# Kernel tuning notes

Hardware: AMD Instinct MI355X
Metric: run time of the kernel (lower is better)

The kernel has to match this reference:

```python
import jax, jax.numpy as jnp
import numpy as np

D_MODEL = 1024
N_HEADS = 16
D_HEAD = D_MODEL // N_HEADS
RANK = 256
N_COMPRESS = 64
N_EXPAND = 64
N_KNOWLEDGE = 4096
K_COMPRESS = 16
K_EXPAND = 8
K_KNOW = 8


def setup_inputs() -> dict:
    key = jax.random.key(0)
    ks = jax.random.split(key, 13)
    B, S = 8, 1024
    x = jax.random.normal(ks[0], (B, S, D_MODEL), dtype=jnp.float32)
    u = jax.random.uniform(ks[1], (B, S), dtype=jnp.float32)
    importance = u / jnp.sum(u, axis=-1, keepdims=True)  # token importance weights
    s = 0.02
    compress_w = jax.random.normal(ks[2], (N_COMPRESS, D_MODEL)) * s
    expQ_w = jax.random.normal(ks[3], (N_EXPAND, D_MODEL)) * s
    expK_w = jax.random.normal(ks[4], (N_EXPAND, D_MODEL)) * s
    expV_w = jax.random.normal(ks[5], (N_EXPAND, D_MODEL)) * s
    memory_w = jax.random.normal(ks[6], (N_COMPRESS, D_MODEL)) * s
    compress_neurons = jax.random.normal(ks[7], (N_COMPRESS, D_MODEL, RANK)) / jnp.sqrt(D_MODEL)
    expand_pool = jax.random.normal(ks[8], (N_EXPAND, RANK, D_MODEL)) / jnp.sqrt(RANK)
    knowledge_K = jax.random.normal(ks[9], (N_KNOWLEDGE, RANK)) * s
    knowledge_V = jax.random.normal(ks[10], (N_KNOWLEDGE, D_MODEL)) * s
    Wo = jax.random.normal(ks[11], (D_MODEL, D_MODEL)) / jnp.sqrt(D_MODEL)
    return dict(x=x, importance=importance, compress_w=compress_w, expQ_w=expQ_w,
                expK_w=expK_w, expV_w=expV_w, memory_w=memory_w,
                compress_neurons=compress_neurons, expand_pool=expand_pool,
                knowledge_K=knowledge_K, knowledge_V=knowledge_V, Wo=Wo)


def _route(x, importance, w_lin, k):
    # softmax router pref [B,S,N], importance-weighted sum -> [B,N], renorm, top-k renorm
    pref = jax.nn.softmax(jnp.einsum('bsd,nd->bsn', x, w_lin), axis=-1)
    w = jnp.einsum('bs,bsn->bn', importance, pref)
    w = w / (jnp.sum(w, axis=-1, keepdims=True) + 1e-8)
    tw, ti = jax.lax.top_k(w, k)
    tw = tw / (jnp.sum(tw, axis=-1, keepdims=True) + 1e-8)
    return tw, ti


def _forward(x, importance, compress_w, expQ_w, expK_w, expV_w, memory_w,
             compress_neurons, expand_pool, knowledge_K, knowledge_V, Wo):
    B, S, D = x.shape
    # ---- attention routing ----
    cw, ci = _route(x, importance, compress_w, K_COMPRESS)
    shared_c = jnp.einsum('bk,bkdr->bdr', cw, compress_neurons[ci])  # [B,D,R]
    h = jnp.einsum('bsd,bdr->bsr', x, shared_c)                      # [B,S,R]

    def expand(w_lin):
        ew, ei = _route(x, importance, w_lin, K_EXPAND)
        shared = jnp.einsum('bk,bkrd->brd', ew, expand_pool[ei])     # [B,R,D]
        return jnp.einsum('bsr,brd->bsd', h, shared)                 # [B,S,D]

    Q, K, V = expand(expQ_w), expand(expK_w), expand(expV_w)
    Qh = Q.reshape(B, S, N_HEADS, D_HEAD).transpose(0, 2, 1, 3)
    Kh = K.reshape(B, S, N_HEADS, D_HEAD).transpose(0, 2, 1, 3)
    Vh = V.reshape(B, S, N_HEADS, D_HEAD).transpose(0, 2, 1, 3)
    scores = jnp.einsum('bhqd,bhkd->bhqk', Qh, Kh) / jnp.sqrt(jnp.float32(D_HEAD))
    causal = jnp.tril(jnp.ones((S, S), dtype=bool))
    scores = jnp.where(causal, scores, jnp.float32(-1e30))
    attn = jax.nn.softmax(scores, axis=-1)
    out = jnp.einsum('bhqk,bhkd->bhqd', attn, Vh)
    out = out.transpose(0, 2, 1, 3).reshape(B, S, D)
    attn_out = jnp.einsum('bsd,ed->bse', out, Wo)

    # ---- memory routing (knowledge lookup) ----
    mw, mi = _route(x, importance, memory_w, K_COMPRESS)
    shared_m = jnp.einsum('bk,bkdr->bdr', mw, compress_neurons[mi])
    hm = jnp.einsum('bsd,bdr->bsr', x, shared_m)                     # [B,S,R]
    kscores = jnp.einsum('bsr,nr->bsn', hm, knowledge_K) / jnp.sqrt(jnp.float32(RANK))
    top_s, top_i = jax.lax.top_k(kscores, K_KNOW)                    # [B,S,k]
    p = jax.nn.softmax(top_s, axis=-1)
    mem_out = jnp.einsum('bsk,bskd->bsd', p, knowledge_V[top_i])

    return attn_out + mem_out


def reference(x, importance, compress_w, expQ_w, expK_w, expV_w, memory_w,
              compress_neurons, expand_pool, knowledge_K, knowledge_V, Wo):
    return _forward(x, importance, compress_w, expQ_w, expK_w, expV_w, memory_w,
                    compress_neurons, expand_pool, knowledge_K, knowledge_V, Wo)
```

## Files before the change

### kernel.cpp

```cpp
#include <hip/hip_runtime.h>

#define Bn   8
#define Sn   1024
#define Dn   1024
#define Rn   256
#define NHn  16
#define DHn  64
#define NKn  4096
#define TOK  (Bn*Sn)
#define EPE  (Dn*Rn)
#define TDN  3072
#define BPAD 44

typedef __attribute__((ext_vector_type(8))) short short8;
typedef __attribute__((ext_vector_type(4))) short short4v;
typedef __attribute__((ext_vector_type(4))) float f32x4;
typedef __attribute__((ext_vector_type(4))) unsigned short ushort4v;
typedef unsigned short ush;

__device__ inline ush f2bf(float f) {
    union { float f; unsigned u; } v; v.f = f;
    unsigned r = v.u + 0x7fffu + ((v.u >> 16) & 1u);
    return (ush)(r >> 16);
}
__device__ inline float bf2f(ush h) {
    union { unsigned u; float f; } v; v.u = ((unsigned)h) << 16;
    return v.f;
}
__device__ inline void f2bf_split(float f, ush& hi, ush& lo) {
    hi = f2bf(f);
    lo = f2bf(f - bf2f(hi));
}
__device__ inline short8 cat8(short4v a, short4v b) {
    short8 r;
    r[0]=a[0]; r[1]=a[1]; r[2]=a[2]; r[3]=a[3];
    r[4]=b[0]; r[5]=b[1]; r[6]=b[2]; r[7]=b[3];
    return r;
}

__global__ __launch_bounds__(256) void convert3(
    const float* __restrict__ s0, ush* __restrict__ h0, ush* __restrict__ l0, long long n40,
    const float* __restrict__ s1, ush* __restrict__ h1, ush* __restrict__ l1, long long n41,
    const float* __restrict__ s2, ush* __restrict__ h2, ush* __restrict__ l2, long long n42)
{
    long long i = (long long)blockIdx.x*256 + threadIdx.x;
    const float* s; ush* h; ush* l;
    if (i < n40) { s = s0; h = h0; l = l0; }
    else if (i < n40 + n41) { i -= n40; s = s1; h = h1; l = l1; }
    else { i -= n40 + n41; if (i >= n42) return; s = s2; h = h2; l = l2; }
    float4 f = *(const float4*)&s[i*4];
    float vals[4] = {f.x, f.y, f.z, f.w};
    ushort4v hv, lv;
#pragma unroll
    for (int e = 0; e < 4; ++e) { ush a, b2; f2bf_split(vals[e], a, b2); hv[e] = a; lv[e] = b2; }
    *(ushort4v*)&h[i*4] = hv;
    *(ushort4v*)&l[i*4] = lv;
}

__global__ __launch_bounds__(256) void convert_w5(
    const float* __restrict__ w0, const float* __restrict__ w1,
    const float* __restrict__ w2, const float* __restrict__ w3,
    const float* __restrict__ w4, ush* __restrict__ hi, ush* __restrict__ lo)
{
    int y = blockIdx.y;
    const float* srcs[5] = {w0, w1, w2, w3, w4};
    const float* s = srcs[y];
    long long i = (long long)blockIdx.x*256 + threadIdx.x;
    float4 f = *(const float4*)&s[i*4];
    float vals[4] = {f.x, f.y, f.z, f.w};
    ushort4v hv, lv;
#pragma unroll
    for (int e = 0; e < 4; ++e) { ush a, b2; f2bf_split(vals[e], a, b2); hv[e] = a; lv[e] = b2; }
    size_t dst = (size_t)y*64*Dn + i*4;
    *(ushort4v*)&hi[dst] = hv;
    *(ushort4v*)&lo[dst] = lv;
}

__global__ __launch_bounds__(256) void gemm_pre(
    const ush* __restrict__ Ahi, const ush* __restrict__ Alo,
    const ush* __restrict__ Bhi, const ush* __restrict__ Blo,
    void* __restrict__ C0, void* __restrict__ C1,
    int M, int N, int K, long long sA, long long sB, long long sC,
    float alpha, int bTrans, int passes, int outMode, int gridSwap)
{
    Ahi += (size_t)blockIdx.z * sA;
    if (Alo) Alo += (size_t)blockIdx.z * sA;
    Bhi += (size_t)blockIdx.z * sB;
    if (Blo) Blo += (size_t)blockIdx.z * sB;
    __shared__ __align__(16) ush AsH[128][40];
    __shared__ __align__(16) ush AsL[128][40];
    __shared__ __align__(16) ush BsH[64][BPAD];
    __shared__ __align__(16) ush BsL[64][BPAD];
    int tid = threadIdx.x;
    int wave = tid >> 6, lane = tid & 63;
    int lr = lane & 15, lg = lane >> 4;
    int wm = (wave >> 1)*64, wn = (wave & 1)*32;
    int row0 = (gridSwap ? blockIdx.x : blockIdx.y)*128;
    int col0 = (gridSwap ? blockIdx.y : blockIdx.x)*64;

    f32x4 acc[4][2];
#pragma unroll
    for (int i = 0; i < 4; ++i)
#pragma unroll
        for (int j = 0; j < 2; ++j) acc[i][j] = (f32x4){0.f,0.f,0.f,0.f};

    for (int k0 = 0; k0 < K; k0 += 32) {
        __syncthreads();
#pragma unroll
        for (int g = 0; g < 2; ++g) {
            int idx = tid + g*256;
            int m2 = idx >> 2, kk = (idx & 3)*8;
            size_t so = (size_t)(row0 + m2)*K + k0 + kk;
            *(short8*)&AsH[m2][kk] = *(const short8*)&Ahi[so];
            if (passes >= 2) *(short8*)&AsL[m2][kk] = *(const short8*)&Alo[so];
        }
        if (!bTrans) {
            int n2 = tid >> 2, kk = (tid & 3)*8;
            size_t so = (size_t)(col0 + n2)*K + k0 + kk;
            *(short4v*)&BsH[n2][kk]     = *(const short4v*)&Bhi[so];
            *(short4v*)&BsH[n2][kk + 4] = *(const short4v*)&Bhi[so + 4];
            if (passes >= 3) {
                *(short4v*)&BsL[n2][kk]     = *(const short4v*)&Blo[so];
                *(short4v*)&BsL[n2][kk + 4] = *(const short4v*)&Blo[so + 4];
            }
        } else {
            int kk = tid >> 3, n0 = (tid & 7)*8;
            size_t so = (size_t)(k0 + kk)*N + col0 + n0;
            short8 wh = *(const short8*)&Bhi[so];
#pragma unroll
            for (int e = 0; e < 8; ++e) BsH[n0+e][kk] = (ush)wh[e];
            if (passes >= 3) {
                short8 wl = *(const short8*)&Blo[so];
#pragma unroll
                for (int e = 0; e < 8; ++e) BsL[n0+e][kk] = (ush)wl[e];
            }
        }
        __syncthreads();
        short8 afH[4], bfH[2];
#pragma unroll
        for (int i = 0; i < 4; ++i) afH[i] = *(const short8*)&AsH[wm + i*16 + lr][lg*8];
#pragma unroll
        for (int j = 0; j < 2; ++j)
            bfH[j] = cat8(*(const short4v*)&BsH[wn + j*16 + lr][lg*8],
                          *(const short4v*)&BsH[wn + j*16 + lr][lg*8 + 4]);
#pragma unroll
        for (int i = 0; i < 4; ++i)
#pragma unroll
            for (int j = 0; j < 2; ++j)
                acc[i][j] = __builtin_amdgcn_mfma_f32_16x16x32_bf16(afH[i], bfH[j], acc[i][j], 0, 0, 0);
        if (passes >= 2) {
            short8 afL[4];
#pragma unroll
            for (int i = 0; i < 4; ++i) afL[i] = *(const short8*)&AsL[wm + i*16 + lr][lg*8];
#pragma unroll
            for (int i = 0; i < 4; ++i)
#pragma unroll
                for (int j = 0; j < 2; ++j)
                    acc[i][j] = __builtin_amdgcn_mfma_f32_16x16x32_bf16(afL[i], bfH[j], acc[i][j], 0, 0, 0);
        }
        if (passes >= 3) {
            short8 bfL[2];
#pragma unroll
            for (int j = 0; j < 2; ++j)
                bfL[j] = cat8(*(const short4v*)&BsL[wn + j*16 + lr][lg*8],
                              *(const short4v*)&BsL[wn + j*16 + lr][lg*8 + 4]);
#pragma unroll
            for (int i = 0; i < 4; ++i)
#pragma unroll
                for (int j = 0; j < 2; ++j)
                    acc[i][j] = __builtin_amdgcn_mfma_f32_16x16x32_bf16(afH[i], bfL[j], acc[i][j], 0, 0, 0);
        }
    }
#pragma unroll
    for (int i = 0; i < 4; ++i)
#pragma unroll
        for (int j = 0; j < 2; ++j)
#pragma unroll
            for (int r = 0; r < 4; ++r) {
                size_t eo = (size_t)(row0 + wm + i*16 + lg*4 + r)*N + col0 + wn + j*16 + lr;
                float val = acc[i][j][r] * alpha;
                if (outMode == 0) {
                    ((float*)C0 + (size_t)blockIdx.z*sC)[eo] = val;
                } else if (outMode == 1) {
                    ((ush*)C0 + (size_t)blockIdx.z*sC)[eo] = f2bf(val);
                } else {
                    ush h, l; f2bf_split(val, h, l);
                    ((ush*)C0 + (size_t)blockIdx.z*sC)[eo] = h;
                    ((ush*)C1 + (size_t)blockIdx.z*sC)[eo] = l;
                }
            }
}

__global__ __launch_bounds__(256) void gemm64(
    const ush* __restrict__ Ahi, const ush* __restrict__ Alo,
    const ush* __restrict__ Bhi, const ush* __restrict__ Blo,
    void* __restrict__ C0, void* __restrict__ C1,
    void* __restrict__ C2, void* __restrict__ C3,
    int N, int K, long long sA, long long sB, long long sCL, long long sCR,
    float alpha, int bTrans, int passes, int mode)
{
    Ahi += (size_t)blockIdx.z * sA;
    if (Alo) Alo += (size_t)blockIdx.z * sA;
    Bhi += (size_t)blockIdx.z * sB;
    if (Blo) Blo += (size_t)blockIdx.z * sB;
    __shared__ __align__(16) ush AsH[64][40];
    __shared__ __align__(16) ush AsL[64][40];
    __shared__ __align__(16) ush BsH[64][BPAD];
    __shared__ __align__(16) ush BsL[64][BPAD];
    int tid = threadIdx.x;
    int wave = tid >> 6, lane = tid & 63;
    int lr = lane & 15, lg = lane >> 4;
    int wm = (wave >> 1)*32, wn = (wave & 1)*32;
    int row0 = blockIdx.y*64, col0 = blockIdx.x*64;

    f32x4 acc[2][2];
#pragma unroll
    for (int i = 0; i < 2; ++i)
#pragma unroll
        for (int j = 0; j < 2; ++j) acc[i][j] = (f32x4){0.f,0.f,0.f,0.f};

    for (int k0 = 0; k0 < K; k0 += 32) {
        __syncthreads();
        {
            int m2 = tid >> 2, kk = (tid & 3)*8;
            size_t so = (size_t)(row0 + m2)*K + k0 + kk;
            *(short8*)&AsH[m2][kk] = *(const short8*)&Ahi[so];
            if (passes >= 2) *(short8*)&AsL[m2][kk] = *(const short8*)&Alo[so];
        }
        if (!bTrans) {
            int n2 = tid >> 2, kk = (tid & 3)*8;
            size_t so = (size_t)(col0 + n2)*K + k0 + kk;
            *(short4v*)&BsH[n2][kk]     = *(const short4v*)&Bhi[so];
            *(short4v*)&BsH[n2][kk + 4] = *(const short4v*)&Bhi[so + 4];
            if (passes >= 3) {
                *(short4v*)&BsL[n2][kk]     = *(const short4v*)&Blo[so];
                *(short4v*)&BsL[n2][kk + 4] = *(const short4v*)&Blo[so + 4];
            }
        } else {
            int kk = tid >> 3, n0 = (tid & 7)*8;
            size_t so = (size_t)(k0 + kk)*N + col0 + n0;
            short8 wh = *(const short8*)&Bhi[so];
#pragma unroll
            for (int e = 0; e < 8; ++e) BsH[n0+e][kk] = (ush)wh[e];
            if (passes >= 3) {
                short8 wl = *(const short8*)&Blo[so];
#pragma unroll
                for (int e = 0; e < 8; ++e) BsL[n0+e][kk] = (ush)wl[e];
            }
        }
        __syncthreads();
        short8 afH[2], bfH[2];
#pragma unroll
        for (int i = 0; i < 2; ++i) afH[i] = *(const short8*)&AsH[wm + i*16 + lr][lg*8];
#pragma unroll
        for (int j = 0; j < 2; ++j)
            bfH[j] = cat8(*(const short4v*)&BsH[wn + j*16 + lr][lg*8],
                          *(const short4v*)&BsH[wn + j*16 + lr][lg*8 + 4]);
#pragma unroll
        for (int i = 0; i < 2; ++i)
#pragma unroll
            for (int j = 0; j < 2; ++j)
                acc[i][j] = __builtin_amdgcn_mfma_f32_16x16x32_bf16(afH[i], bfH[j], acc[i][j], 0, 0, 0);
        if (passes >= 2) {
            short8 afL[2];
#pragma unroll
            for (int i = 0; i < 2; ++i) afL[i] = *(const short8*)&AsL[wm + i*16 + lr][lg*8];
#pragma unroll
            for (int i = 0; i < 2; ++i)
#pragma unroll
                for (int j = 0; j < 2; ++j)
                    acc[i][j] = __builtin_amdgcn_mfma_f32_16x16x32_bf16(afL[i], bfH[j], acc[i][j], 0, 0, 0);
        }
        if (passes >= 3) {
            short8 bfL[2];
#pragma unroll
            for (int j = 0; j < 2; ++j)
                bfL[j] = cat8(*(const short4v*)&BsL[wn + j*16 + lr][lg*8],
                              *(const short4v*)&BsL[wn + j*16 + lr][lg*8 + 4]);
#pragma unroll
            for (int i = 0; i < 2; ++i)
#pragma unroll
                for (int j = 0; j < 2; ++j)
                    acc[i][j] = __builtin_amdgcn_mfma_f32_16x16x32_bf16(afH[i], bfL[j], acc[i][j], 0, 0, 0);
        }
    }
    int Nh = N >> 1;
#pragma unroll
    for (int i = 0; i < 2; ++i)
#pragma unroll
        for (int j = 0; j < 2; ++j)
#pragma unroll
            for (int r = 0; r < 4; ++r) {
                int grow = row0 + wm + i*16 + lg*4 + r;
                int gcol = col0 + wn + j*16 + lr;
                float val = acc[i][j][r] * alpha;
                if (mode == 0) {
                    ((float*)C0 + (size_t)blockIdx.z*sCL)[(size_t)grow*N + gcol] = val;
                } else {
                    if (gcol < Nh) {
                        ush h, l; f2bf_split(val, h, l);
                        size_t eo = (size_t)blockIdx.z*sCL + (size_t)grow*Nh + gcol;
                        ((ush*)C0)[eo] = h;
                        ((ush*)C1)[eo] = l;
                    } else {
                        size_t eo = (size_t)blockIdx.z*sCR + (size_t)grow*Nh + (gcol - Nh);
                        ((float*)C2)[eo] = val;
                        ((ush*)C3)[eo] = f2bf(val);
                    }
                }
            }
}

__global__ __launch_bounds__(256) void router_post(
    const float* __restrict__ logits, const float* __restrict__ imp,
    float* __restrict__ partial)
{
    int blk = blockIdx.x;
    int chunk = blk & 3, b = (blk >> 2) & 7, r = blk >> 5;
    int tid = threadIdx.x, lane = tid & 63, wv = tid >> 6;
    float acc = 0.f;
    for (int i = wv; i < 256; i += 4) {
        int t = b*1024 + chunk*256 + i;
        float lgv = logits[(size_t)t*320 + r*64 + lane];
        float mx = lgv;
        for (int off = 32; off >= 1; off >>= 1) mx = fmaxf(mx, __shfl_xor(mx, off));
        float e = __expf(lgv - mx);
        float s = e;
        for (int off = 32; off >= 1; off >>= 1) s += __shfl_xor(s, off);
        acc += imp[t] * e / s;
    }
    __shared__ float red[4][64];
    red[wv][lane] = acc;
    __syncthreads();
    if (tid < 64)
        partial[((size_t)(r*8 + b)*4 + chunk)*64 + tid]
            = red[0][tid] + red[1][tid] + red[2][tid] + red[3][tid];
}

__global__ void topk_router(const float* __restrict__ partial,
                            float* __restrict__ tw, int* __restrict__ ti)
{
    int rb = blockIdx.x;
    int r  = rb >> 3;
    int lane = threadIdx.x;
    float v = partial[((size_t)rb*4 + 0)*64 + lane] + partial[((size_t)rb*4 + 1)*64 + lane]
            + partial[((size_t)rb*4 + 2)*64 + lane] + partial[((size_t)rb*4 + 3)*64 + lane];
    float s = v;
    for (int off = 32; off >= 1; off >>= 1) s += __shfl_xor(s, off);
    v = v / (s + 1e-8f);
    int k = (r == 0 || r == 4) ? 16 : 8;
    __shared__ float tv[16];
    __shared__ int   tix[16];
    float cur = v;
    for (int it = 0; it < k; ++it) {
        float bv = cur; int bi = lane;
        for (int off = 32; off >= 1; off >>= 1) {
            float ov = __shfl_xor(bv, off);
            int   oi = __shfl_xor(bi, off);
            if (ov > bv || (ov == bv && oi < bi)) { bv = ov; bi = oi; }
        }
        if (bi == lane) cur = -1e30f;
        if (lane == 0) { tv[it] = bv; tix[it] = bi; }
    }
    __syncthreads();
    float s2 = 0.f;
    for (int i = 0; i < k; ++i) s2 += tv[i];
    float inv = 1.f / (s2 + 1e-8f);
    if (lane < k) {
        tw[(size_t)rb*16 + lane] = tv[lane] * inv;
        ti[(size_t)rb*16 + lane] = tix[lane];
    }
}

__global__ __launch_bounds__(256) void combine_split(
    const float* __restrict__ table, const float* __restrict__ tw,
    const int* __restrict__ ti, ush* __restrict__ outhi,
    ush* __restrict__ outlo, int k, int nInner, int rowStride, int colOff,
    long long sOut)
{
    int b = blockIdx.y;
    size_t e = ((size_t)blockIdx.x*256 + threadIdx.x)*4;
    float4 acc = {0.f, 0.f, 0.f, 0.f};
    for (int i = 0; i < k; ++i) {
        float w = tw[b*16 + i];
        int  idx = ti[b*16 + i];
        float4 t = *(const float4*)&table[(size_t)idx*EPE + e];
        acc.x += w*t.x; acc.y += w*t.y; acc.z += w*t.z; acc.w += w*t.w;
    }
    float vals[4] = {acc.x, acc.y, acc.z, acc.w};
    ushort4v h, l;
#pragma unroll
    for (int i = 0; i < 4; ++i) {
        ush a, b2; f2bf_split(vals[i], a, b2);
        h[i] = a; l[i] = b2;
    }
    int row = (int)(e / nInner), col = (int)(e % nInner);
    size_t dst = (size_t)b*sOut + (size_t)row*rowStride + colOff + col;
    *(ushort4v*)&outhi[dst] = h;
    *(ushort4v*)&outlo[dst] = l;
}

#define PADK 72

__global__ __launch_bounds__(256, 4) void attn_mfma_kernel(
    const ush* __restrict__ QKV,
    ush* __restrict__ Ohi, ush* __restrict__ Olo)
{
    int aa = blockIdx.x;
    int hh = blockIdx.y, b = blockIdx.z;
    int qt0 = aa, qt1 = 15 - aa;
    int tid  = threadIdx.x;
    int wave = tid >> 6, lane = tid & 63;
    int lr = lane & 15, lg = lane >> 4;

    __shared__ __align__(16) ush Kt[64][PADK];
    __shared__ __align__(16) ush Vt[64][PADK];
    __shared__ __align__(16) ush Pt[64][PADK];

    const ush* Qr0 = QKV + ((size_t)b*Sn + (size_t)qt0*64 + wave*16 + lr)*TDN + hh*64;
    const ush* Qr1 = QKV + ((size_t)b*Sn + (size_t)qt1*64 + wave*16 + lr)*TDN + hh*64;
    short8 q0a = *(const short8*)&Qr0[lg*8];
    short8 q0b = *(const short8*)&Qr0[32 + lg*8];
    short8 q1a = *(const short8*)&Qr1[lg*8];
    short8 q1b = *(const short8*)&Qr1[32 + lg*8];

    f32x4 o0[4], o1[4];
    float m0[4], l0[4], m1[4], l1[4];
#pragma unroll
    for (int ct = 0; ct < 4; ++ct) {
        o0[ct] = (f32x4){0.f,0.f,0.f,0.f};
        o1[ct] = (f32x4){0.f,0.f,0.f,0.f};
    }
#pragma unroll
    for (int r = 0; r < 4; ++r) {
        m0[r] = -1e30f; l0[r] = 0.f;
        m1[r] = -1e30f; l1[r] = 0.f;
    }

    auto process = [&](short8 qa, short8 qb, f32x4 (&o)[4],
                       float (&m)[4], float (&l)[4], int qt, int kt) {
        f32x4 s[4];
#pragma unroll
        for (int ct = 0; ct < 4; ++ct) {
            s[ct] = (f32x4){0.f,0.f,0.f,0.f};
            short8 k0 = *(const short8*)&Kt[ct*16 + lr][lg*8];
            short8 k1 = *(const short8*)&Kt[ct*16 + lr][32 + lg*8];
            s[ct] = __builtin_amdgcn_mfma_f32_16x16x32_bf16(qa, k0, s[ct], 0, 0, 0);
            s[ct] = __builtin_amdgcn_mfma_f32_16x16x32_bf16(qb, k1, s[ct], 0, 0, 0);
        }
        float mx[4] = {-1e30f,-1e30f,-1e30f,-1e30f};
        int qg0 = qt*64 + wave*16 + lg*4;
#pragma unroll
        for (int ct = 0; ct < 4; ++ct) {
            int kvg = kt*64 + ct*16 + lr;
#pragma unroll
            for (int r = 0; r < 4; ++r) {
                float v = s[ct][r] * 0.125f;
                if (kt == qt && kvg > qg0 + r) v = -1e30f;
                s[ct][r] = v;
                mx[r] = fmaxf(mx[r], v);
            }
        }
#pragma unroll
        for (int r = 0; r < 4; ++r) {
            mx[r] = fmaxf(mx[r], __shfl_xor(mx[r], 1));
            mx[r] = fmaxf(mx[r], __shfl_xor(mx[r], 2));
            mx[r] = fmaxf(mx[r], __shfl_xor(mx[r], 4));
            mx[r] = fmaxf(mx[r], __shfl_xor(mx[r], 8));
        }
        float corr[4], ps[4] = {0.f,0.f,0.f,0.f};
#pragma unroll
        for (int r = 0; r < 4; ++r) {
            float mn = fmaxf(m[r], mx[r]);
            corr[r] = __expf(m[r] - mn);
            m[r] = mn;
        }
#pragma unroll
        for (int ct = 0; ct < 4; ++ct)
#pragma unroll
            for (int r = 0; r < 4; ++r) {
                float e = __expf(s[ct][r] - m[r]);
                s[ct][r] = e;
                ps[r] += e;
            }
#pragma unroll
        for (int r = 0; r < 4; ++r) {
            ps[r] += __shfl_xor(ps[r], 1);
            ps[r] += __shfl_xor(ps[r], 2);
            ps[r] += __shfl_xor(ps[r], 4);
            ps[r] += __shfl_xor(ps[r], 8);
            l[r] = l[r]*corr[r] + ps[r];
#pragma unroll
            for (int ct = 0; ct < 4; ++ct) o[ct][r] *= corr[r];
        }
#pragma unroll
        for (int ct = 0; ct < 4; ++ct)
#pragma unroll
            for (int r = 0; r < 4; ++r)
                Pt[wave*16 + lg*4 + r][ct*16 + lr] = f2bf(s[ct][r]);
        short8 pa0 = *(const short8*)&Pt[wave*16 + lr][lg*8];
        short8 pa1 = *(const short8*)&Pt[wave*16 + lr][32 + lg*8];
#pragma unroll
        for (int ct = 0; ct < 4; ++ct) {
            short8 v0 = *(const short8*)&Vt[ct*16 + lr][lg*8];
            short8 v1 = *(const short8*)&Vt[ct*16 + lr][32 + lg*8];
            o[ct] = __builtin_amdgcn_mfma_f32_16x16x32_bf16(pa0, v0, o[ct], 0, 0, 0);
            o[ct] = __builtin_amdgcn_mfma_f32_16x16x32_bf16(pa1, v1, o[ct], 0, 0, 0);
        }
    };

    for (int kt = 0; kt <= qt1; ++kt) {
        __syncthreads();
        const ush* Kb = QKV + ((size_t)b*Sn + (size_t)kt*64)*TDN + 1024 + hh*64;
        const ush* Vb = QKV + ((size_t)b*Sn + (size_t)kt*64)*TDN + 2048 + hh*64;
#pragma unroll
        for (int it2 = 0; it2 < 2; ++it2) {
            int idx = tid + it2*256;
            int kv = idx >> 3, d0 = (idx & 7)*8;
            *(short8*)&Kt[kv][d0] = *(const short8*)&Kb[(size_t)kv*TDN + d0];
        }
#pragma unroll
        for (int it2 = 0; it2 < 2; ++it2) {
            int idx = tid + it2*256;
            int kv = idx & 63, d0 = (idx >> 6)*8;
            short8 w = *(const short8*)&Vb[(size_t)kv*TDN + d0];
#pragma unroll
            for (int e = 0; e < 8; ++e) Vt[d0+e][kv] = (ush)w[e];
        }
        __syncthreads();

        if (kt <= qt0) process(q0a, q0b, o0, m0, l0, qt0, kt);
        process(q1a, q1b, o1, m1, l1, qt1, kt);
    }

    {
        size_t base = ((size_t)b*Sn + (size_t)qt0*64 + wave*16 + lg*4)*Dn + hh*64 + lr;
#pragma unroll
        for (int r = 0; r < 4; ++r) {
            float inv = 1.f / l0[r];
#pragma unroll
            for (int ct = 0; ct < 4; ++ct) {
                float val = o0[ct][r] * inv;
                ush h, lo2; f2bf_split(val, h, lo2);
                Ohi[base + (size_t)r*Dn + ct*16] = h;
                Olo[base + (size_t)r*Dn + ct*16] = lo2;
            }
        }
    }
    {
        size_t base = ((size_t)b*Sn + (size_t)qt1*64 + wave*16 + lg*4)*Dn + hh*64 + lr;
#pragma unroll
        for (int r = 0; r < 4; ++r) {
            float inv = 1.f / l1[r];
#pragma unroll
            for (int ct = 0; ct < 4; ++ct) {
                float val = o1[ct][r] * inv;
                ush h, lo2; f2bf_split(val, h, lo2);
                Ohi[base + (size_t)r*Dn + ct*16] = h;
                Olo[base + (size_t)r*Dn + ct*16] = lo2;
            }
        }
    }
}

__global__ __launch_bounds__(256) void mem_topk_wave(
    const ush* __restrict__ ksc,
    const float* __restrict__ hm,
    const float* __restrict__ kK,
    const float* __restrict__ kV,
    float* __restrict__ out, int tok0)
{
    int wave = threadIdx.x >> 6, lane = threadIdx.x & 63;
    int t = blockIdx.x*4 + wave;
    const ush* row = ksc + (size_t)t*NKn;

    float v[64];
    float lmax = -3e38f;
#pragma unroll
    for (int j8 = 0; j8 < 8; ++j8) {
        short8 w = *(const short8*)&row[lane*64 + j8*8];
#pragma unroll
        for (int e = 0; e < 8; ++e) {
            float f = bf2f((ush)w[e]);
            v[j8*8+e] = f;
            lmax = fmaxf(lmax, f);
        }
    }

    float sv = lmax;
#pragma unroll
    for (int k = 2; k <= 64; k <<= 1) {
#pragma unroll
        for (int j = k >> 1; j >= 1; j >>= 1) {
            float ov = __shfl_xor(sv, j);
            bool keepLarger = (((lane & j) == 0) == ((lane & k) == 0));
            float mx = fmaxf(sv, ov), mn = fminf(sv, ov);
            sv = keepLarger ? mx : mn;
        }
    }
    float T = __shfl(sv, 15);

    __shared__ float s_cv[4][64];
    __shared__ int   s_cix[4][64];
    __shared__ float s_cs[4][16];
    __shared__ int   s_tix[4][16];

    int cnt = 0;
#pragma unroll
    for (int j = 0; j < 64; ++j) cnt += (v[j] >= T) ? 1 : 0;
    int pre = cnt;
#pragma unroll
    for (int off2 = 1; off2 < 64; off2 <<= 1) {
        int og = __shfl_up(pre, off2);
        if (lane >= off2) pre += og;
    }
    int C = __shfl(pre, 63);
    int base = pre - cnt;

    if (C <= 64) {
        int pos = base;
#pragma unroll
        for (int j = 0; j < 64; ++j) {
            if (v[j] >= T) {
                s_cv[wave][pos] = v[j];
                s_cix[wave][pos] = lane*64 + j;
                ++pos;
            }
        }
        float cv2 = (lane < C) ? s_cv[wave][lane] : -3e38f;
        int   cix = (lane < C) ? s_cix[wave][lane] : 0x7fffffff;
#pragma unroll
        for (int k = 2; k <= 64; k <<= 1) {
#pragma unroll
            for (int j = k >> 1; j >= 1; j >>= 1) {
                float ov = __shfl_xor(cv2, j);
                int   oi = __shfl_xor(cix, j);
                bool amLarger = (cv2 > ov) || (cv2 == ov && cix < oi);
                bool keepLarger = (((lane & j) == 0) == ((lane & k) == 0));
                if (amLarger != keepLarger) { cv2 = ov; cix = oi; }
            }
        }
        if (lane < 16) s_tix[wave][lane] = cix;
    } else {
        for (int it = 0; it < 16; ++it) {
            float bv = -3e38f; int bi = 0x7fffffff;
#pragma unroll
            for (int j = 0; j < 64; ++j) {
                int n = lane*64 + j;
                if (v[j] > bv || (v[j] == bv && n < bi)) { bv = v[j]; bi = n; }
            }
#pragma unroll
            for (int off2 = 32; off2 >= 1; off2 >>= 1) {
                float ov = __shfl_xor(bv, off2);
                int   oi = __shfl_xor(bi, off2);
                if (ov > bv || (ov == bv && oi < bi)) { bv = ov; bi = oi; }
            }
            if (lane == 0) s_tix[wave][it] = bi;
#pragma unroll
            for (int j = 0; j < 64; ++j)
                if (lane*64 + j == bi) v[j] = -3e38f;
        }
    }

    int c = lane >> 2, q = lane & 3;
    int kidx = s_tix[wave][c];
    const float* kr = kK + (size_t)kidx*Rn;
    const float* hr = hm + (size_t)(tok0 + t)*Rn;
    float d = 0.f;
#pragma unroll
    for (int j4 = 0; j4 < 16; ++j4) {
        float4 a  = *(const float4*)&hr[q*64 + j4*4];
        float4 bb = *(const float4*)&kr[q*64 + j4*4];
        d += a.x*bb.x + a.y*bb.y + a.z*bb.z + a.w*bb.w;
    }
    d += __shfl_xor(d, 1);
    d += __shfl_xor(d, 2);
    if (q == 0) s_cs[wave][c] = d * 0.0625f;

    float cv = (lane < 16) ? s_cs[wave][lane] : -3e38f;
    int   ck = (lane < 16) ? s_tix[wave][lane] : 0x7fffffff;
    float sv8[8]; int si[8];
#pragma unroll
    for (int it = 0; it < 8; ++it) {
        float bv = cv; int bk = ck;
#pragma unroll
        for (int off2 = 32; off2 >= 1; off2 >>= 1) {
            float ov = __shfl_xor(bv, off2);
            int   ok = __shfl_xor(bk, off2);
            if (ov > bv || (ov == bv && ok < bk)) { bv = ov; bk = ok; }
        }
        sv8[it] = bv; si[it] = bk;
        if (ck == bk) cv = -3e38f;
    }

    float mxv = sv8[0];
#pragma unroll
    for (int kx = 1; kx < 8; ++kx) mxv = fmaxf(mxv, sv8[kx]);
    float p[8]; float sum = 0.f;
#pragma unroll
    for (int kx = 0; kx < 8; ++kx) { p[kx] = __expf(sv8[kx] - mxv); sum += p[kx]; }
    float invs = 1.f / sum;
    float4 acc0 = {0,0,0,0}, acc1 = {0,0,0,0}, acc2 = {0,0,0,0}, acc3 = {0,0,0,0};
#pragma unroll
    for (int kx = 0; kx < 8; ++kx) {
        float pk = p[kx]*invs;
        const float* vp = kV + (size_t)si[kx]*Dn + lane*16;
        float4 v0 = *(const float4*)(vp + 0);
        float4 v1 = *(const float4*)(vp + 4);
        float4 v2 = *(const float4*)(vp + 8);
        float4 v3 = *(const float4*)(vp + 12);
        acc0.x += pk*v0.x; acc0.y += pk*v0.y; acc0.z += pk*v0.z; acc0.w += pk*v0.w;
        acc1.x += pk*v1.x; acc1.y += pk*v1.y; acc1.z += pk*v1.z; acc1.w += pk*v1.w;
        acc2.x += pk*v2.x; acc2.y += pk*v2.y; acc2.z += pk*v2.z; acc2.w += pk*v2.w;
        acc3.x += pk*v3.x; acc3.y += pk*v3.y; acc3.z += pk*v3.z; acc3.w += pk*v3.w;
    }
    float* op = out + (size_t)(tok0 + t)*Dn + lane*16;
    float4 c0 = *(const float4*)(op + 0);
    float4 c1 = *(const float4*)(op + 4);
    float4 c2 = *(const float4*)(op + 8);
    float4 c3 = *(const float4*)(op + 12);
    c0.x+=acc0.x; c0.y+=acc0.y; c0.z+=acc0.z; c0.w+=acc0.w;
    c1.x+=acc1.x; c1.y+=acc1.y; c1.z+=acc1.z; c1.w+=acc1.w;
    c2.x+=acc2.x; c2.y+=acc2.y; c2.z+=acc2.z; c2.w+=acc2.w;
    c3.x+=acc3.x; c3.y+=acc3.y; c3.z+=acc3.z; c3.w+=acc3.w;
    *(float4*)(op + 0)  = c0;
    *(float4*)(op + 4)  = c1;
    *(float4*)(op + 8)  = c2;
    *(float4*)(op + 12) = c3;
}

extern "C" void kernel_launch(void* const* d_in, const int* in_sizes, int n_in,
                              void* d_out, int out_size, void* d_ws, size_t ws_size,
                              hipStream_t stream)
{
    const float* x          = (const float*)d_in[0];
    const float* imp        = (const float*)d_in[1];
    const float* compress_w = (const float*)d_in[2];
    const float* expQ_w     = (const float*)d_in[3];
    const float* expK_w     = (const float*)d_in[4];
    const float* expV_w     = (const float*)d_in[5];
    const float* memory_w   = (const float*)d_in[6];
    const float* neurons    = (const float*)d_in[7];
    const float* pool       = (const float*)d_in[8];
    const float* kK         = (const float*)d_in[9];
    const float* kV         = (const float*)d_in[10];
    const float* Wo         = (const float*)d_in[11];
    float* out = (float*)d_out;

    char* ws = (char*)d_ws;
    size_t off = 0;
    auto alloc = [&](size_t bytes) {
        size_t o = off; off = (off + bytes + 255) & ~(size_t)255; return (void*)(ws + o);
    };
    ush* xqh    = (ush*)alloc((size_t)TOK*Dn*2);
    ush* xql    = (ush*)alloc((size_t)TOK*Dn*2);
    ush* wcatqh = (ush*)alloc((size_t)320*Dn*2);
    ush* wcatql = (ush*)alloc((size_t)320*Dn*2);
    ush* Woqh   = (ush*)alloc((size_t)Dn*Dn*2);
    ush* Woql   = (ush*)alloc((size_t)Dn*Dn*2);
    ush* kKqh   = (ush*)alloc((size_t)NKn*Rn*2);
    ush* kKql   = (ush*)alloc((size_t)NKn*Rn*2);
    float* logits  = (float*)alloc((size_t)TOK*320*4);
    float* partial = (float*)alloc((size_t)40*4*64*4);
    float* tw      = (float*)alloc((size_t)5*Bn*16*4);
    int*   ti      = (int*)  alloc((size_t)5*Bn*16*4);
    ush* hhmBh = (ush*)alloc((size_t)Bn*2*EPE*2);
    ush* hhmBl = (ush*)alloc((size_t)Bn*2*EPE*2);
    ush* qkvBh = (ush*)alloc((size_t)Bn*3*EPE*2);
    ush* qkvBl = (ush*)alloc((size_t)Bn*3*EPE*2);
    ush* hqh   = (ush*)alloc((size_t)TOK*Rn*2);
    ush* hql   = (ush*)alloc((size_t)TOK*Rn*2);
    float* hm  = (float*)alloc((size_t)TOK*Rn*4);
    ush* hmqh  = (ush*)alloc((size_t)TOK*Rn*2);
    ush* QKVb  = (ush*)alloc((size_t)TOK*TDN*2);
    ush* Obqh  = (ush*)alloc((size_t)TOK*Dn*2);
    ush* Obql  = (ush*)alloc((size_t)TOK*Dn*2);
    ush* ksc = QKVb;
    (void)ws_size; (void)in_sizes; (void)n_in; (void)out_size;

    convert3<<<10240, 256, 0, stream>>>(
        x, xqh, xql, (long long)TOK*Dn/4,
        Wo, Woqh, Woql, (long long)Dn*Dn/4,
        kK, kKqh, kKql, (long long)NKn*Rn/4);
    convert_w5<<<dim3(64, 5), 256, 0, stream>>>(
        compress_w, expQ_w, expK_w, expV_w, memory_w, wcatqh, wcatql);

    gemm64<<<dim3(5, 128, 1), 256, 0, stream>>>(
        xqh, xql, wcatqh, wcatql, logits, nullptr, nullptr, nullptr,
        320, Dn, 0LL, 0LL, 0LL, 0LL, 1.f, 0 , 3, 0);
    router_post<<<160, 256, 0, stream>>>(logits, imp, partial);
    topk_router<<<40, 64, 0, stream>>>(partial, tw, ti);

    dim3 cgrid(EPE/1024, Bn);
    combine_split<<<cgrid, 256, 0, stream>>>(neurons, tw + 0*128, ti + 0*128,
        hhmBh, hhmBl, 16, 256, 512, 0,   (long long)2*EPE);
    combine_split<<<cgrid, 256, 0, stream>>>(neurons, tw + 4*128, ti + 4*128,
        hhmBh, hhmBl, 16, 256, 512, 256, (long long)2*EPE);
    combine_split<<<cgrid, 256, 0, stream>>>(pool, tw + 1*128, ti + 1*128,
        qkvBh, qkvBl, 8, 1024, TDN, 0,    (long long)3*EPE);
    combine_split<<<cgrid, 256, 0, stream>>>(pool, tw + 2*128, ti + 2*128,
        qkvBh, qkvBl, 8, 1024, TDN, 1024, (long long)3*EPE);
    combine_split<<<cgrid, 256, 0, stream>>>(pool, tw + 3*128, ti + 3*128,
        qkvBh, qkvBl, 8, 1024, TDN, 2048, (long long)3*EPE);

    gemm64<<<dim3(8, 16, Bn), 256, 0, stream>>>(
        xqh, xql, hhmBh, hhmBl, hqh, hql, hm, hmqh,
        512, Dn, (long long)Sn*Dn, (long long)2*EPE,
        (long long)Sn*Rn, (long long)Sn*Rn, 1.f, 1 , 3, 1);

    gemm_pre<<<dim3(TDN/64, Sn/128, Bn), 256, 0, stream>>>(
        hqh, hql, qkvBh, qkvBl, QKVb, nullptr,
        Sn, TDN, Rn, (long long)Sn*Rn, (long long)3*EPE, (long long)Sn*TDN,
        1.f, 1 , 3, 1, 0);

    attn_mfma_kernel<<<dim3(8, NHn, Bn), 256, 0, stream>>>(QKVb, Obqh, Obql);

    gemm_pre<<<dim3(TOK/128, Dn/64, 1), 256, 0, stream>>>(
        Obqh, Obql, Woqh, Woql, out, nullptr,
        TOK, Dn, Dn, 0LL, 0LL, 0LL, 1.f, 0 , 2, 0, 1 );

    for (int c = 0; c < 2; ++c) {
        gemm_pre<<<dim3(NKn/64, 4096/128, 1), 256, 0, stream>>>(
            hmqh + (size_t)c*4096*Rn, nullptr, kKqh, nullptr, ksc, nullptr,
            4096, NKn, Rn, 0LL, 0LL, 0LL, 0.0625f, 0 , 1, 1 , 0);
        mem_topk_wave<<<1024, 256, 0, stream>>>(ksc, hm, kK, kV, out, c*4096);
    }
}
```

Baseline: 624.1 us.

## Merge combine launches, unchunk memory top-k, add MFMA priority hints in attention

The five combine_split launches become one combine_all kernel, which picks its table, output buffer and offsets from blockIdx.z. The two-chunk loop of knowledge-score GEMM plus top-k is replaced by one GEMM over all tokens and one larger mem_topk_wave launch, removing launches and improving device fill. The attention kernel wraps its QK and PV MFMA sequences in s_setprio so the matrix work is favoured over other waves. The unchunked score buffer is now twice as large while still aliasing the QKV workspace, so it may spill past that allocation into the buffers that follow it.

```diff
diff --git a/kernel.cpp b/kernel.cpp
--- a/kernel.cpp
+++ b/kernel.cpp
@@ -372,18 +372,37 @@
     }
 }
 
-__global__ __launch_bounds__(256) void combine_split(
-    const float* __restrict__ table, const float* __restrict__ tw,
-    const int* __restrict__ ti, ush* __restrict__ outhi,
-    ush* __restrict__ outlo, int k, int nInner, int rowStride, int colOff,
-    long long sOut)
-{
+__global__ __launch_bounds__(256) void combine_all(
+    const float* __restrict__ neurons, const float* __restrict__ pool,
+    const float* __restrict__ tw, const int* __restrict__ ti,
+    ush* __restrict__ hhmBh, ush* __restrict__ hhmBl,
+    ush* __restrict__ qkvBh, ush* __restrict__ qkvBl)
+{
+    int seg = blockIdx.z;
     int b = blockIdx.y;
+    const float* table;
+    int twIdx, k, nInner, rowStride, colOff;
+    ush *outhi, *outlo;
+    long long sOut;
+    if (seg < 2) {
+        table = neurons; k = 16; nInner = 256; rowStride = 512;
+        twIdx = (seg == 0) ? 0 : 4;
+        colOff = (seg == 0) ? 0 : 256;
+        outhi = hhmBh; outlo = hhmBl; sOut = (long long)2*EPE;
+    } else {
+        table = pool; k = 8; nInner = 1024; rowStride = TDN;
+        twIdx = seg - 1;
+        colOff = (seg - 2)*1024;
+        outhi = qkvBh; outlo = qkvBl; sOut = (long long)3*EPE;
+    }
+    const float* twp = tw + (size_t)(twIdx*Bn + b)*16;
+    const int*   tip = ti + (size_t)(twIdx*Bn + b)*16;
+
     size_t e = ((size_t)blockIdx.x*256 + threadIdx.x)*4;
     float4 acc = {0.f, 0.f, 0.f, 0.f};
     for (int i = 0; i < k; ++i) {
-        float w = tw[b*16 + i];
-        int  idx = ti[b*16 + i];
+        float w = twp[i];
+        int  idx = tip[i];
         float4 t = *(const float4*)&table[(size_t)idx*EPE + e];
         acc.x += w*t.x; acc.y += w*t.y; acc.z += w*t.z; acc.w += w*t.w;
     }
@@ -440,6 +459,7 @@
     auto process = [&](short8 qa, short8 qb, f32x4 (&o)[4],
                        float (&m)[4], float (&l)[4], int qt, int kt) {
         f32x4 s[4];
+        __builtin_amdgcn_s_setprio(1);
 #pragma unroll
         for (int ct = 0; ct < 4; ++ct) {
             s[ct] = (f32x4){0.f,0.f,0.f,0.f};
@@ -448,6 +468,7 @@
             s[ct] = __builtin_amdgcn_mfma_f32_16x16x32_bf16(qa, k0, s[ct], 0, 0, 0);
             s[ct] = __builtin_amdgcn_mfma_f32_16x16x32_bf16(qb, k1, s[ct], 0, 0, 0);
         }
+        __builtin_amdgcn_s_setprio(0);
         float mx[4] = {-1e30f,-1e30f,-1e30f,-1e30f};
         int qg0 = qt*64 + wave*16 + lg*4;
 #pragma unroll
@@ -500,6 +521,7 @@
                 Pt[wave*16 + lg*4 + r][ct*16 + lr] = f2bf(s[ct][r]);
         short8 pa0 = *(const short8*)&Pt[wave*16 + lr][lg*8];
         short8 pa1 = *(const short8*)&Pt[wave*16 + lr][32 + lg*8];
+        __builtin_amdgcn_s_setprio(1);
 #pragma unroll
         for (int ct = 0; ct < 4; ++ct) {
             short8 v0 = *(const short8*)&Vt[ct*16 + lr][lg*8];
@@ -507,6 +529,7 @@
             o[ct] = __builtin_amdgcn_mfma_f32_16x16x32_bf16(pa0, v0, o[ct], 0, 0, 0);
             o[ct] = __builtin_amdgcn_mfma_f32_16x16x32_bf16(pa1, v1, o[ct], 0, 0, 0);
         }
+        __builtin_amdgcn_s_setprio(0);
     };
 
     for (int kt = 0; kt <= qt1; ++kt) {
@@ -568,7 +591,7 @@
     const float* __restrict__ hm,
     const float* __restrict__ kK,
     const float* __restrict__ kV,
-    float* __restrict__ out, int tok0)
+    float* __restrict__ out)
 {
     int wave = threadIdx.x >> 6, lane = threadIdx.x & 63;
     int t = blockIdx.x*4 + wave;
@@ -665,7 +688,7 @@
     int c = lane >> 2, q = lane & 3;
     int kidx = s_tix[wave][c];
     const float* kr = kK + (size_t)kidx*Rn;
-    const float* hr = hm + (size_t)(tok0 + t)*Rn;
+    const float* hr = hm + (size_t)t*Rn;
     float d = 0.f;
 #pragma unroll
     for (int j4 = 0; j4 < 16; ++j4) {
@@ -714,7 +737,7 @@
         acc2.x += pk*v2.x; acc2.y += pk*v2.y; acc2.z += pk*v2.z; acc2.w += pk*v2.w;
         acc3.x += pk*v3.x; acc3.y += pk*v3.y; acc3.z += pk*v3.z; acc3.w += pk*v3.w;
     }
-    float* op = out + (size_t)(tok0 + t)*Dn + lane*16;
+    float* op = out + (size_t)t*Dn + lane*16;
     float4 c0 = *(const float4*)(op + 0);
     float4 c1 = *(const float4*)(op + 4);
     float4 c2 = *(const float4*)(op + 8);
@@ -791,17 +814,8 @@
     router_post<<<160, 256, 0, stream>>>(logits, imp, partial);
     topk_router<<<40, 64, 0, stream>>>(partial, tw, ti);
 
-    dim3 cgrid(EPE/1024, Bn);
-    combine_split<<<cgrid, 256, 0, stream>>>(neurons, tw + 0*128, ti + 0*128,
-        hhmBh, hhmBl, 16, 256, 512, 0,   (long long)2*EPE);
-    combine_split<<<cgrid, 256, 0, stream>>>(neurons, tw + 4*128, ti + 4*128,
-        hhmBh, hhmBl, 16, 256, 512, 256, (long long)2*EPE);
-    combine_split<<<cgrid, 256, 0, stream>>>(pool, tw + 1*128, ti + 1*128,
-        qkvBh, qkvBl, 8, 1024, TDN, 0,    (long long)3*EPE);
-    combine_split<<<cgrid, 256, 0, stream>>>(pool, tw + 2*128, ti + 2*128,
-        qkvBh, qkvBl, 8, 1024, TDN, 1024, (long long)3*EPE);
-    combine_split<<<cgrid, 256, 0, stream>>>(pool, tw + 3*128, ti + 3*128,
-        qkvBh, qkvBl, 8, 1024, TDN, 2048, (long long)3*EPE);
+    combine_all<<<dim3(EPE/1024, Bn, 5), 256, 0, stream>>>(
+        neurons, pool, tw, ti, hhmBh, hhmBl, qkvBh, qkvBl);
 
     gemm64<<<dim3(8, 16, Bn), 256, 0, stream>>>(
         xqh, xql, hhmBh, hhmBl, hqh, hql, hm, hmqh,
@@ -819,10 +833,8 @@
         Obqh, Obql, Woqh, Woql, out, nullptr,
         TOK, Dn, Dn, 0LL, 0LL, 0LL, 1.f, 0 , 2, 0, 1 );
 
-    for (int c = 0; c < 2; ++c) {
-        gemm_pre<<<dim3(NKn/64, 4096/128, 1), 256, 0, stream>>>(
-            hmqh + (size_t)c*4096*Rn, nullptr, kKqh, nullptr, ksc, nullptr,
-            4096, NKn, Rn, 0LL, 0LL, 0LL, 0.0625f, 0 , 1, 1 , 0);
-        mem_topk_wave<<<1024, 256, 0, stream>>>(ksc, hm, kK, kV, out, c*4096);
-    }
-}
+    gemm_pre<<<dim3(NKn/64, TOK/128, 1), 256, 0, stream>>>(
+        hmqh, nullptr, kKqh, nullptr, ksc, nullptr,
+        TOK, NKn, Rn, 0LL, 0LL, 0LL, 0.0625f, 0 , 1, 1 , 0);
+    mem_topk_wave<<<2048, 256, 0, stream>>>(ksc, hm, kK, kV, out);
+}
```

After: 600.9 us, median of 3. -3.7%, faster.
